# Performance work log

Hardware: AMD Instinct MI355X
Metric: run time of the kernel (lower is better)

## Reference

```python
import jax, jax.numpy as jnp
import numpy as np

N = 50000      # nodes
E = 800000     # edges (before self loops)
RNA, SS, H, G = 645, 6, 128, 200
EPS = 1e-5

def setup_inputs() -> dict:
    key = jax.random.key(0)
    ks = jax.random.split(key, 16)
    def rn(k, shape, s=0.05):
        return jax.random.normal(k, shape, jnp.float32) * s
    return {
        "rna_embeddings": jax.random.normal(ks[0], (N, RNA), jnp.float32),
        "ss_emb": jax.random.normal(ks[1], (N, SS), jnp.float32),
        "edge_index": jax.random.randint(ks[2], (2, E), 0, N),
        "batch": jnp.sort(jax.random.randint(ks[3], (N,), 0, G)),
        "W_fuse": rn(ks[4], (RNA + SS, H)), "b_fuse": jnp.zeros((H,), jnp.float32),
        "ln1_g": jnp.ones((H,), jnp.float32), "ln1_b": jnp.zeros((H,), jnp.float32),
        "W_gat": rn(ks[5], (H, H)), "att_src": rn(ks[6], (H,)), "att_dst": rn(ks[7], (H,)),
        "b_gat": jnp.zeros((H,), jnp.float32),
        "gn_w": jnp.ones((H,), jnp.float32), "gn_b": jnp.zeros((H,), jnp.float32), "gn_ms": jnp.ones((H,), jnp.float32),
        "W_gate": rn(ks[8], (2 * H, H)), "b_gate": jnp.zeros((H,), jnp.float32),
        "W_head": rn(ks[9], (H, H)), "b_head": jnp.zeros((H,), jnp.float32),
        "ln2_g": jnp.ones((H,), jnp.float32), "ln2_b": jnp.zeros((H,), jnp.float32),
        "W_fc1": rn(ks[10], (H, H // 2)), "b_fc1": jnp.zeros((H // 2,), jnp.float32),
        "ln3_g": jnp.ones((H // 2,), jnp.float32), "ln3_b": jnp.zeros((H // 2,), jnp.float32),
        "W_fc2": rn(ks[11], (H // 2, 1)), "b_fc2": jnp.zeros((1,), jnp.float32),
    }

def _ln(x, g, b):
    m = jnp.mean(x, -1, keepdims=True)
    v = jnp.mean(jnp.square(x - m), -1, keepdims=True)
    return (x - m) * jax.lax.rsqrt(v + EPS) * g + b

def _graphnorm(x, batch, w, b, ms):
    cnt = jax.ops.segment_sum(jnp.ones((x.shape[0], 1), x.dtype), batch, num_segments=G)
    mean = jax.ops.segment_sum(x, batch, num_segments=G) / jnp.maximum(cnt, 1.0)
    out = x - ms * mean[batch]
    var = jax.ops.segment_sum(jnp.square(out), batch, num_segments=G) / jnp.maximum(cnt, 1.0)
    std = jnp.sqrt(var + EPS)
    return w * out / std[batch] + b

def _gat(x, src, dst, W, a_src, a_dst, bias):
    xw = x @ W                                     # [N,H]
    e = (xw @ a_src)[src] + (xw @ a_dst)[dst]      # per-edge score
    e = jax.nn.leaky_relu(e, 0.2)
    m = jax.ops.segment_max(e, dst, num_segments=N)  # every dst has a self loop
    e = jnp.exp(e - m[dst])
    s = jax.ops.segment_sum(e, dst, num_segments=N)
    alpha = e / (s[dst] + 1e-16)
    return jax.ops.segment_sum(alpha[:, None] * xw[src], dst, num_segments=N) + bias

def reference(rna_embeddings, ss_emb, edge_index, batch,
              W_fuse, b_fuse, ln1_g, ln1_b,
              W_gat, att_src, att_dst, b_gat,
              gn_w, gn_b, gn_ms,
              W_gate, b_gate, W_head, b_head, ln2_g, ln2_b,
              W_fc1, b_fc1, ln3_g, ln3_b, W_fc2, b_fc2):
    loop = jnp.arange(N)
    src = jnp.concatenate([edge_index[0], loop])   # PyG GATConv add_self_loops=True
    dst = jnp.concatenate([edge_index[1], loop])
    h = jax.nn.relu(_ln(jnp.concatenate([rna_embeddings, ss_emb], -1) @ W_fuse + b_fuse, ln1_g, ln1_b))
    h_res = h
    h = jax.nn.relu(_graphnorm(_gat(h, src, dst, W_gat, att_src, att_dst, b_gat), batch, gn_w, gn_b, gn_ms))
    h1 = h
    h = jax.nn.relu(_graphnorm(_gat(h1, src, dst, W_gat, att_src, att_dst, b_gat), batch, gn_w, gn_b, gn_ms))
    h2 = h + h_res
    gate = jax.nn.sigmoid(jnp.concatenate([h1, h2], -1) @ W_gate + b_gate)
    h = gate * h1 + (1.0 - gate) * h2
    h = jax.nn.relu(_ln(h @ W_head + b_head, ln2_g, ln2_b))
    h = jax.nn.relu(_ln(h @ W_fc1 + b_fc1, ln3_g, ln3_b))
    return (h @ W_fc2 + b_fc2)[:, 0]
```

## Files before the change

### kernel.cpp

```cpp
#include <hip/hip_runtime.h>
#include <hip/hip_bf16.h>
#include <math.h>

#define NN 50000
#define EE 800000
#define RNA_D 645
#define KFUSE 651
#define KPACK 704
#define HD 128
#define GG 200
#define SAK 72
#define HGS 136

typedef __attribute__((ext_vector_type(8))) short shortx8;
typedef __attribute__((ext_vector_type(4))) float floatx4;

__device__ __forceinline__ float lrelu(float x){ return x >= 0.f ? x : 0.2f*x; }
__device__ __forceinline__ short f2bf(float x){
  union { __hip_bfloat16 h; short s; } u; u.h = __float2bfloat16(x); return u.s;
}
__device__ __forceinline__ float bf2f(short s){
  union { float f; unsigned u; } c; c.u = ((unsigned)(unsigned short)s) << 16; return c.f;
}
__device__ __forceinline__ float2 upk(unsigned u){
  union { float f; unsigned v; } a, b;
  a.v = u << 16; b.v = u & 0xffff0000u;
  return make_float2(a.f, b.f);
}

__global__ void hist_gstart_kernel(const int* __restrict__ dst, int* __restrict__ deg,
                                   const int* __restrict__ batch, int* __restrict__ gstart){
  int e = blockIdx.x*256 + threadIdx.x;
  if (e < EE) atomicAdd(&deg[dst[e]], 1);
  if (e < NN){
    int g = batch[e];
    if (e == 0){ for (int gg=0; gg<=g; ++gg) gstart[gg] = 0; }
    else { int gp = batch[e-1]; for (int gg=gp+1; gg<=g; ++gg) gstart[gg] = e; }
    if (e == NN-1){ for (int gg=g+1; gg<=GG; ++gg) gstart[gg] = NN; }
  }
}
__global__ void scan1_kernel(const int* __restrict__ deg, int* __restrict__ row_start,
                             int* __restrict__ blocksum){
  __shared__ int s[256];
  int i = blockIdx.x*256 + threadIdx.x;
  int v = (i < NN) ? deg[i] : 0;
  s[threadIdx.x] = v;
  __syncthreads();
  for (int off=1; off<256; off<<=1){
    int t = (threadIdx.x >= off) ? s[threadIdx.x-off] : 0;
    __syncthreads();
    s[threadIdx.x] += t;
    __syncthreads();
  }
  if (i < NN) row_start[i] = s[threadIdx.x] - v;
  if (threadIdx.x == 255) blocksum[blockIdx.x] = s[255];
}
__global__ void scan2_kernel(int* __restrict__ blocksum, int nb){
  __shared__ int s[256];
  int v = (threadIdx.x < nb) ? blocksum[threadIdx.x] : 0;
  s[threadIdx.x] = v;
  __syncthreads();
  for (int off=1; off<256; off<<=1){
    int t = (threadIdx.x >= off) ? s[threadIdx.x-off] : 0;
    __syncthreads();
    s[threadIdx.x] += t;
    __syncthreads();
  }
  blocksum[threadIdx.x] = s[threadIdx.x] - v;
}
__global__ void scan3_kernel(int* __restrict__ row_start, const int* __restrict__ blocksum,
                             int* __restrict__ cursor){
  int i = blockIdx.x*256 + threadIdx.x;
  if (i < NN){
    int v = row_start[i] + blocksum[blockIdx.x];
    row_start[i] = v;
    cursor[i] = v;
  }
  if (i == 0) row_start[NN] = EE;
}
__global__ void scatter_kernel(const int* __restrict__ srcl, const int* __restrict__ dstl,
                               int* __restrict__ cursor, int* __restrict__ csr_src){
  int e = blockIdx.x*256 + threadIdx.x;
  if (e >= EE) return;
  int d = dstl[e];
  int slot = atomicAdd(&cursor[d], 1);
  csr_src[slot] = srcl[e];
}

__global__ void wprep_all_kernel(const float* __restrict__ Wf, const float* __restrict__ Wg,
                                 const float* __restrict__ Wgt, const float* __restrict__ Wh,
                                 const float* __restrict__ W1,
                                 short* __restrict__ Tf, short* __restrict__ Tg,
                                 short* __restrict__ Tgt, short* __restrict__ Th,
                                 short* __restrict__ T1){
  int idx = blockIdx.x*256 + threadIdx.x;
  const int S0=128*KPACK, S1=128*128, S2=128*256, S3=128*128, S4=64*128;
  if (idx < S0){ int n=idx/KPACK, k=idx-n*KPACK; Tf[idx]=f2bf(k<KFUSE ? Wf[k*128+n] : 0.f); return; }
  idx -= S0;
  if (idx < S1){ int n=idx>>7, k=idx&127; Tg[idx]=f2bf(Wg[k*128+n]); return; }
  idx -= S1;
  if (idx < S2){ int n=idx>>8, k=idx&255; Tgt[idx]=f2bf(Wgt[k*128+n]); return; }
  idx -= S2;
  if (idx < S3){ int n=idx>>7, k=idx&127; Th[idx]=f2bf(Wh[k*128+n]); return; }
  idx -= S3;
  if (idx < S4){ int n=idx>>7, k=idx&127; T1[idx]=f2bf(W1[k*64+n]); return; }
}

__launch_bounds__(256)
__global__ void fuse_xw_kernel(const float* __restrict__ rna, const float* __restrict__ ss,
                               const short* __restrict__ Wtf, const float* __restrict__ bfu,
                               const float* __restrict__ g1, const float* __restrict__ b1,
                               const short* __restrict__ Wtg,
                               const float* __restrict__ as_, const float* __restrict__ ad_,
                               float* __restrict__ hout, short* __restrict__ xwb,
                               float* __restrict__ es, float* __restrict__ ed){
  __shared__ short sA[128*SAK];
  __shared__ short sB[128*SAK];
  __shared__ short hA[128*HGS];
  const int tid  = threadIdx.x;
  const int wave = tid >> 6, lane = tid & 63;
  const int quad = lane >> 4, l16 = lane & 15;
  const int rowBase = blockIdx.x * 128;
  const int srow = tid >> 1, shalf = tid & 1;
  const int sgr = rowBase + srow;

  floatx4 acc[2][8];
  #pragma unroll
  for (int t=0;t<2;++t)
    #pragma unroll
    for (int ct=0;ct<8;++ct)
      #pragma unroll
      for (int j=0;j<4;++j) acc[t][ct][j] = 0.f;

  for (int k0 = 0; k0 < KPACK; k0 += 64){
    {
      short tmp[32];
      if (sgr < NN && k0 < 640){
        const float* rrow = rna + (size_t)sgr*RNA_D + k0 + shalf*32;
        #pragma unroll
        for (int j=0;j<32;++j) tmp[j] = f2bf(rrow[j]);
      } else if (sgr < NN){
        int cb = k0 + shalf*32;
        #pragma unroll
        for (int j=0;j<32;++j){
          int c = cb + j;
          float v = 0.f;
          if (c < RNA_D) v = rna[(size_t)sgr*RNA_D + c];
          else if (c < KFUSE) v = ss[sgr*6 + (c - RNA_D)];
          tmp[j] = f2bf(v);
        }
      } else {
        #pragma unroll
        for (int j=0;j<32;++j) tmp[j] = 0;
      }
      #pragma unroll
      for (int q8=0;q8<4;++q8)
        *(shortx8*)&sA[srow*SAK + shalf*32 + q8*8] = *(shortx8*)&tmp[q8*8];
    }
    {
      int col = tid >> 1, kb = k0 + (tid&1)*32;
      #pragma unroll
      for (int q8=0;q8<4;++q8)
        *(shortx8*)&sB[col*SAK + (tid&1)*32 + q8*8] = *(const shortx8*)&Wtf[(size_t)col*KPACK + kb + q8*8];
    }
    __syncthreads();
    #pragma unroll
    for (int ks=0; ks<2; ++ks){
      int kb = ks*32 + quad*8;
      shortx8 af0 = *(const shortx8*)&sA[(wave*32 +      l16)*SAK + kb];
      shortx8 af1 = *(const shortx8*)&sA[(wave*32 + 16 + l16)*SAK + kb];
      #pragma unroll
      for (int ct=0; ct<8; ++ct){
        shortx8 bf = *(const shortx8*)&sB[(ct*16 + l16)*SAK + kb];
        acc[0][ct] = __builtin_amdgcn_mfma_f32_16x16x32_bf16(af0, bf, acc[0][ct], 0,0,0);
        acc[1][ct] = __builtin_amdgcn_mfma_f32_16x16x32_bf16(af1, bf, acc[1][ct], 0,0,0);
      }
    }
    __syncthreads();
  }

  {
    float biasv[8], gv[8], bv[8];
    #pragma unroll
    for (int ct=0;ct<8;++ct){
      biasv[ct] = bfu[ct*16+l16]; gv[ct] = g1[ct*16+l16]; bv[ct] = b1[ct*16+l16];
    }
    #pragma unroll
    for (int t=0;t<2;++t)
      #pragma unroll
      for (int i=0;i<4;++i){
        int row = wave*32 + t*16 + quad*4 + i;
        int gr = rowBase + row;
        float v[8]; float s=0.f, q=0.f;
        #pragma unroll
        for (int ct=0;ct<8;++ct){
          v[ct] = acc[t][ct][i] + biasv[ct];
          s += v[ct]; q = fmaf(v[ct], v[ct], q);
        }
        #pragma unroll
        for (int off=1; off<16; off<<=1){ s += __shfl_xor(s,off); q += __shfl_xor(q,off); }
        float mean = s * (1.f/128.f);
        float inv  = rsqrtf(q*(1.f/128.f) - mean*mean + 1e-5f);
        #pragma unroll
        for (int ct=0;ct<8;++ct){
          float o = fmaxf((v[ct]-mean)*inv*gv[ct] + bv[ct], 0.f);
          if (gr < NN) hout[(size_t)gr*HD + ct*16 + l16] = o;
          hA[row*HGS + ct*16 + l16] = f2bf(o);
        }
      }
  }
  __syncthreads();

  floatx4 acc2[2][8];
  #pragma unroll
  for (int t=0;t<2;++t)
    #pragma unroll
    for (int ct=0;ct<8;++ct)
      #pragma unroll
      for (int j=0;j<4;++j) acc2[t][ct][j] = 0.f;

  for (int c2=0; c2<2; ++c2){
    {
      int col = tid >> 1, kb2 = c2*64 + (tid&1)*32;
      #pragma unroll
      for (int q8=0;q8<4;++q8)
        *(shortx8*)&sB[col*SAK + (tid&1)*32 + q8*8] = *(const shortx8*)&Wtg[(size_t)col*HD + kb2 + q8*8];
    }
    __syncthreads();
    #pragma unroll
    for (int ks=0; ks<2; ++ks){
      int kg = c2*64 + ks*32 + quad*8;
      int kk = ks*32 + quad*8;
      shortx8 af0 = *(const shortx8*)&hA[(wave*32 +      l16)*HGS + kg];
      shortx8 af1 = *(const shortx8*)&hA[(wave*32 + 16 + l16)*HGS + kg];
      #pragma unroll
      for (int ct=0; ct<8; ++ct){
        shortx8 bf = *(const shortx8*)&sB[(ct*16 + l16)*SAK + kk];
        acc2[0][ct] = __builtin_amdgcn_mfma_f32_16x16x32_bf16(af0, bf, acc2[0][ct], 0,0,0);
        acc2[1][ct] = __builtin_amdgcn_mfma_f32_16x16x32_bf16(af1, bf, acc2[1][ct], 0,0,0);
      }
    }
    __syncthreads();
  }

  {
    float asv[8], adv[8];
    #pragma unroll
    for (int ct=0;ct<8;++ct){ asv[ct] = as_[ct*16+l16]; adv[ct] = ad_[ct*16+l16]; }
    #pragma unroll
    for (int t=0;t<2;++t)
      #pragma unroll
      for (int i=0;i<4;++i){
        int gr = rowBase + wave*32 + t*16 + quad*4 + i;
        float s=0.f, d=0.f;
        #pragma unroll
        for (int ct=0;ct<8;++ct){
          float v = acc2[t][ct][i];
          s = fmaf(v, asv[ct], s); d = fmaf(v, adv[ct], d);
          if (gr < NN) xwb[(size_t)gr*HD + ct*16 + l16] = f2bf(v);
        }
        #pragma unroll
        for (int off=1; off<16; off<<=1){ s += __shfl_xor(s,off); d += __shfl_xor(d,off); }
        if (l16 == 0 && gr < NN){ es[gr] = s; ed[gr] = d; }
      }
  }
}

template<int MODE, int NT, bool GNA>
__launch_bounds__(256)
__global__ void mfma_gemm(const float* __restrict__ A0,
                          const short* __restrict__ Apk,
                          const short* __restrict__ Wt, const float* __restrict__ bias,
                          const float* __restrict__ gw, const float* __restrict__ gb,
                          const float* __restrict__ as_, const float* __restrict__ ad_,
                          const int* __restrict__ batch, const float* __restrict__ gnsh,
                          const float* __restrict__ gnsc, float* __restrict__ side,
                          float* __restrict__ out, short* __restrict__ outb,
                          float* __restrict__ es, float* __restrict__ ed,
                          int K, int Kp){
  __shared__ short sA[128*SAK];
  __shared__ short sB[NT*16*SAK];
  const int tid  = threadIdx.x;
  const int wave = tid >> 6, lane = tid & 63;
  const int quad = lane >> 4, l16 = lane & 15;
  const int rowBase = blockIdx.x * 128;
  const int NCOL = NT*16;

  floatx4 acc[2][NT];
  #pragma unroll
  for (int t=0;t<2;++t)
    #pragma unroll
    for (int ct=0;ct<NT;++ct)
      #pragma unroll
      for (int j=0;j<4;++j) acc[t][ct][j] = 0.f;

  const int srow = tid >> 1, shalf = tid & 1;
  const int sgr = rowBase + srow;

  for (int k0 = 0; k0 < K; k0 += 64){
    {
      int kb = k0 + shalf*32;
      short tmp[32];
      if (GNA){
        int g = (sgr < NN) ? batch[sgr] : 0;
        const float* py  = A0 + (size_t)sgr*HD + kb;
        const float* psh = gnsh + g*HD + kb;
        const float* psc = gnsc + g*HD + kb;
        const float* pbb = gb + kb;
        #pragma unroll
        for (int q4=0;q4<8;++q4){
          float4 yv = (sgr < NN) ? *(const float4*)(py + q4*4) : make_float4(0.f,0.f,0.f,0.f);
          float4 sh = *(const float4*)(psh + q4*4);
          float4 sc = *(const float4*)(psc + q4*4);
          float4 bb = *(const float4*)(pbb + q4*4);
          float4 v;
          v.x = fmaxf((yv.x - sh.x)*sc.x + bb.x, 0.f);
          v.y = fmaxf((yv.y - sh.y)*sc.y + bb.y, 0.f);
          v.z = fmaxf((yv.z - sh.z)*sc.z + bb.z, 0.f);
          v.w = fmaxf((yv.w - sh.w)*sc.w + bb.w, 0.f);
          if (sgr < NN) *(float4*)&side[(size_t)sgr*HD + kb + q4*4] = v;
          tmp[q4*4+0]=f2bf(v.x); tmp[q4*4+1]=f2bf(v.y);
          tmp[q4*4+2]=f2bf(v.z); tmp[q4*4+3]=f2bf(v.w);
        }
      } else {
        const float* p = A0 + (size_t)sgr*HD + kb;
        #pragma unroll
        for (int q4=0;q4<8;++q4){
          float4 f = (sgr < NN) ? *(const float4*)(p + q4*4) : make_float4(0.f,0.f,0.f,0.f);
          tmp[q4*4+0]=f2bf(f.x); tmp[q4*4+1]=f2bf(f.y);
          tmp[q4*4+2]=f2bf(f.z); tmp[q4*4+3]=f2bf(f.w);
        }
      }
      #pragma unroll
      for (int q8=0;q8<4;++q8)
        *(shortx8*)&sA[srow*SAK + shalf*32 + q8*8] = *(shortx8*)&tmp[q8*8];
    }
    {
      int col = tid >> 1, kb = k0 + (tid&1)*32;
      #pragma unroll
      for (int q8=0;q8<4;++q8)
        *(shortx8*)&sB[col*SAK + (tid&1)*32 + q8*8] = *(const shortx8*)&Wt[(size_t)col*Kp + kb + q8*8];
    }
    __syncthreads();
    #pragma unroll
    for (int ks=0; ks<2; ++ks){
      int kb = ks*32 + quad*8;
      shortx8 af0 = *(const shortx8*)&sA[(wave*32 +      l16)*SAK + kb];
      shortx8 af1 = *(const shortx8*)&sA[(wave*32 + 16 + l16)*SAK + kb];
      #pragma unroll
      for (int ct=0; ct<NT; ++ct){
        shortx8 bf = *(const shortx8*)&sB[(ct*16 + l16)*SAK + kb];
        acc[0][ct] = __builtin_amdgcn_mfma_f32_16x16x32_bf16(af0, bf, acc[0][ct], 0,0,0);
        acc[1][ct] = __builtin_amdgcn_mfma_f32_16x16x32_bf16(af1, bf, acc[1][ct], 0,0,0);
      }
    }
    __syncthreads();
  }

  {
    float asv[NT], adv[NT];
    #pragma unroll
    for (int ct=0;ct<NT;++ct){ asv[ct] = as_[ct*16+l16]; adv[ct] = ad_[ct*16+l16]; }
    #pragma unroll
    for (int t=0;t<2;++t)
      #pragma unroll
      for (int i=0;i<4;++i){
        int gr = rowBase + wave*32 + t*16 + quad*4 + i;
        float s=0.f, d=0.f;
        #pragma unroll
        for (int ct=0;ct<NT;++ct){
          float v = acc[t][ct][i];
          s = fmaf(v, asv[ct], s); d = fmaf(v, adv[ct], d);
          if (gr < NN) outb[(size_t)gr*HD + ct*16 + l16] = f2bf(v);
        }
        #pragma unroll
        for (int off=1; off<16; off<<=1){ s += __shfl_xor(s,off); d += __shfl_xor(d,off); }
        if (l16 == 0 && gr < NN){ es[gr] = s; ed[gr] = d; }
      }
  }
}

__launch_bounds__(256)
__global__ void gat_aggregate_kernel(const short* __restrict__ xwb, const float* __restrict__ es,
                                     const float* __restrict__ ed, const int* __restrict__ row_start,
                                     const int* __restrict__ csr_src, const float* __restrict__ bgat,
                                     float* __restrict__ out){
  int gid = blockIdx.x*256 + threadIdx.x;
  int n = gid >> 6, lane = gid & 63;
  if (n >= NN) return;
  int beg = row_start[n], end = row_start[n+1];
  float edn = ed[n];
  float sc_self = lrelu(es[n] + edn);

  int i0 = beg + lane;
  bool v0 = i0 < end;
  int sA = v0 ? csr_src[i0] : 0;
  float eA = v0 ? lrelu(es[sA] + edn) : -3.0e38f;
  float m = fmaxf(sc_self, eA);
  for (int i = beg + 64 + lane; i < end; i += 64)
    m = fmaxf(m, lrelu(es[csr_src[i]] + edn));
  #pragma unroll
  for (int off=1; off<64; off<<=1) m = fmaxf(m, __shfl_xor(m, off));

  float wA = v0 ? __expf(eA - m) : 0.f;
  float wsum_l = wA;
  float wself = __expf(sc_self - m);
  float2 self2 = upk(*(const unsigned*)&xwb[(size_t)n*HD + 2*lane]);
  float a0 = wself*self2.x, a1 = wself*self2.y;

  int deg0 = min(end - beg, 64);
  int j = 0;
  for (; j + 8 <= deg0; j += 8){
    int ss[8]; float ww[8]; unsigned xv[8];
    #pragma unroll
    for (int u=0;u<8;++u){ ss[u]=__shfl(sA,j+u); ww[u]=__shfl(wA,j+u); }
    #pragma unroll
    for (int u=0;u<8;++u) xv[u] = *(const unsigned*)&xwb[(size_t)ss[u]*HD + 2*lane];
    #pragma unroll
    for (int u=0;u<8;++u){ float2 f=upk(xv[u]); a0=fmaf(ww[u],f.x,a0); a1=fmaf(ww[u],f.y,a1); }
  }
  for (; j < deg0; ++j){
    int s=__shfl(sA,j); float w=__shfl(wA,j);
    float2 f = upk(*(const unsigned*)&xwb[(size_t)s*HD + 2*lane]);
    a0=fmaf(w,f.x,a0); a1=fmaf(w,f.y,a1);
  }
  for (int c = beg + 64; c < end; c += 64){
    int i = c + lane;
    bool vb = i < end;
    int sB = vb ? csr_src[i] : 0;
    float wB = vb ? __expf(lrelu(es[sB] + edn) - m) : 0.f;
    wsum_l += wB;
    int degc = min(end - c, 64);
    for (int jj=0; jj<degc; ++jj){
      int s=__shfl(sB,jj); float w=__shfl(wB,jj);
      float2 f = upk(*(const unsigned*)&xwb[(size_t)s*HD + 2*lane]);
      a0=fmaf(w,f.x,a0); a1=fmaf(w,f.y,a1);
    }
  }
  #pragma unroll
  for (int off=1; off<64; off<<=1) wsum_l += __shfl_xor(wsum_l, off);
  float dinv = 1.f/(wsum_l + wself + 1e-16f);
  float2 b2 = *(const float2*)&bgat[2*lane];
  float2 o; o.x = a0*dinv + b2.x; o.y = a1*dinv + b2.y;
  *(float2*)&out[(size_t)n*HD + 2*lane] = o;
}

__launch_bounds__(1024)
__global__ void gn_group_kernel(const float* __restrict__ x, const int* __restrict__ gstart,
                                const float* __restrict__ gnw, const float* __restrict__ gnms,
                                float* __restrict__ shiftv, float* __restrict__ scalev){
  int g = blockIdx.x;
  int n0 = gstart[g], n1 = gstart[g+1];
  int f = threadIdx.x & 127, slot = threadIdx.x >> 7;
  float s = 0.f, q = 0.f;
  for (int n = n0 + slot; n < n1; n += 8){
    float v = x[(size_t)n*HD + f];
    s += v; q = fmaf(v, v, q);
  }
  __shared__ float rs[1024], rq[1024];
  rs[threadIdx.x] = s; rq[threadIdx.x] = q;
  __syncthreads();
  if (threadIdx.x < 512){ rs[threadIdx.x] += rs[threadIdx.x+512]; rq[threadIdx.x] += rq[threadIdx.x+512]; }
  __syncthreads();
  if (threadIdx.x < 256){ rs[threadIdx.x] += rs[threadIdx.x+256]; rq[threadIdx.x] += rq[threadIdx.x+256]; }
  __syncthreads();
  if (threadIdx.x < 128){
    s = rs[threadIdx.x] + rs[threadIdx.x+128];
    q = rq[threadIdx.x] + rq[threadIdx.x+128];
    float c = fmaxf((float)(n1 - n0), 1.f);
    float mean = s / c;
    float ms = gnms[f];
    float var = q/c - mean*mean*ms*(2.f - ms);
    shiftv[g*HD+f] = ms*mean;
    scalev[g*HD+f] = gnw[f] / sqrtf(var + 1e-5f);
  }
}

__launch_bounds__(256)
__global__ void tail_kernel(const float* __restrict__ h1, const float* __restrict__ y2,
                            const float* __restrict__ hres, const int* __restrict__ batch,
                            const float* __restrict__ gnsh, const float* __restrict__ gnsc,
                            const float* __restrict__ gnb,
                            const short* __restrict__ Wt_gate, const float* __restrict__ b_gate,
                            const short* __restrict__ Wt_head, const float* __restrict__ b_head,
                            const float* __restrict__ ln2g, const float* __restrict__ ln2b,
                            const short* __restrict__ Wt_fc1, const float* __restrict__ b_fc1,
                            const float* __restrict__ ln3g, const float* __restrict__ ln3b,
                            const float* __restrict__ W_fc2, const float* __restrict__ b_fc2,
                            float* __restrict__ outp){
  __shared__ short hgL[128*HGS];
  __shared__ short sA[128*SAK];
  __shared__ short sB[128*SAK];
  const int tid = threadIdx.x, wave = tid>>6, lane = tid&63;
  const int quad = lane>>4, l16 = lane&15;
  const int rowBase = blockIdx.x*128;
  const int srow = tid>>1, shalf = tid&1;
  const int sgr = rowBase + srow;

  floatx4 acc[2][8];
  #pragma unroll
  for (int t=0;t<2;++t)
    #pragma unroll
    for (int ct=0;ct<8;++ct)
      #pragma unroll
      for (int j=0;j<4;++j) acc[t][ct][j]=0.f;

  for (int c2=0; c2<4; ++c2){
    int kb = c2*64 + shalf*32;
    short tmp[32];
    if (kb < 128){
      const float* p = h1 + (size_t)sgr*HD + kb;
      #pragma unroll
      for (int q4=0;q4<8;++q4){
        float4 f = (sgr < NN) ? *(const float4*)(p + q4*4) : make_float4(0.f,0.f,0.f,0.f);
        tmp[q4*4+0]=f2bf(f.x); tmp[q4*4+1]=f2bf(f.y);
        tmp[q4*4+2]=f2bf(f.z); tmp[q4*4+3]=f2bf(f.w);
      }
    } else {
      int cb = kb - 128;
      int g = (sgr < NN) ? batch[sgr] : 0;
      const float* py  = y2   + (size_t)sgr*HD + cb;
      const float* ph  = hres + (size_t)sgr*HD + cb;
      const float* psh = gnsh + g*HD + cb;
      const float* psc = gnsc + g*HD + cb;
      const float* pbb = gnb + cb;
      #pragma unroll
      for (int q4=0;q4<8;++q4){
        float4 yv = (sgr < NN) ? *(const float4*)(py + q4*4) : make_float4(0.f,0.f,0.f,0.f);
        float4 hv = (sgr < NN) ? *(const float4*)(ph + q4*4) : make_float4(0.f,0.f,0.f,0.f);
        float4 sh = *(const float4*)(psh + q4*4);
        float4 sc = *(const float4*)(psc + q4*4);
        float4 bb = *(const float4*)(pbb + q4*4);
        float4 v;
        v.x = fmaxf((yv.x - sh.x)*sc.x + bb.x, 0.f) + hv.x;
        v.y = fmaxf((yv.y - sh.y)*sc.y + bb.y, 0.f) + hv.y;
        v.z = fmaxf((yv.z - sh.z)*sc.z + bb.z, 0.f) + hv.z;
        v.w = fmaxf((yv.w - sh.w)*sc.w + bb.w, 0.f) + hv.w;
        tmp[q4*4+0]=f2bf(v.x); tmp[q4*4+1]=f2bf(v.y);
        tmp[q4*4+2]=f2bf(v.z); tmp[q4*4+3]=f2bf(v.w);
      }
      #pragma unroll
      for (int q8=0;q8<4;++q8)
        *(shortx8*)&hgL[srow*HGS + cb + q8*8] = *(shortx8*)&tmp[q8*8];
    }
    #pragma unroll
    for (int q8=0;q8<4;++q8)
      *(shortx8*)&sA[srow*SAK + shalf*32 + q8*8] = *(shortx8*)&tmp[q8*8];
    {
      int col = tid >> 1, kb2 = c2*64 + (tid&1)*32;
      #pragma unroll
      for (int q8=0;q8<4;++q8)
        *(shortx8*)&sB[col*SAK + (tid&1)*32 + q8*8] = *(const shortx8*)&Wt_gate[(size_t)col*256 + kb2 + q8*8];
    }
    __syncthreads();
    #pragma unroll
    for (int ks=0; ks<2; ++ks){
      int kk = ks*32 + quad*8;
      shortx8 af0 = *(const shortx8*)&sA[(wave*32 +      l16)*SAK + kk];
      shortx8 af1 = *(const shortx8*)&sA[(wave*32 + 16 + l16)*SAK + kk];
      #pragma unroll
      for (int ct=0; ct<8; ++ct){
        shortx8 bf = *(const shortx8*)&sB[(ct*16 + l16)*SAK + kk];
        acc[0][ct] = __builtin_amdgcn_mfma_f32_16x16x32_bf16(af0, bf, acc[0][ct], 0,0,0);
        acc[1][ct] = __builtin_amdgcn_mfma_f32_16x16x32_bf16(af1, bf, acc[1][ct], 0,0,0);
      }
    }
    __syncthreads();
  }
  {
    float biasv[8];
    #pragma unroll
    for (int ct=0;ct<8;++ct) biasv[ct] = b_gate[ct*16+l16];
    #pragma unroll
    for (int t=0;t<2;++t)
      #pragma unroll
      for (int i=0;i<4;++i){
        int row = wave*32 + t*16 + quad*4 + i;
        int gr = rowBase + row;
        #pragma unroll
        for (int ct=0;ct<8;++ct){
          int c = ct*16 + l16;
          float g = 1.f/(1.f + __expf(-(acc[t][ct][i] + biasv[ct])));
          float x1 = (gr < NN) ? h1[(size_t)gr*HD + c] : 0.f;
          float x2 = bf2f(hgL[row*HGS + c]);
          hgL[row*HGS + c] = f2bf(g*x1 + (1.f-g)*x2);
        }
      }
  }
  __syncthreads();

  floatx4 acc2[2][8];
  #pragma unroll
  for (int t=0;t<2;++t)
    #pragma unroll
    for (int ct=0;ct<8;++ct)
      #pragma unroll
      for (int j=0;j<4;++j) acc2[t][ct][j]=0.f;
  for (int c2=0;c2<2;++c2){
    {
      int col = tid >> 1, kb2 = c2*64 + (tid&1)*32;
      #pragma unroll
      for (int q8=0;q8<4;++q8)
        *(shortx8*)&sB[col*SAK + (tid&1)*32 + q8*8] = *(const shortx8*)&Wt_head[(size_t)col*128 + kb2 + q8*8];
    }
    __syncthreads();
    #pragma unroll
    for (int ks=0; ks<2; ++ks){
      int kg = c2*64 + ks*32 + quad*8;
      int kk = ks*32 + quad*8;
      shortx8 af0 = *(const shortx8*)&hgL[(wave*32 +      l16)*HGS + kg];
      shortx8 af1 = *(const shortx8*)&hgL[(wave*32 + 16 + l16)*HGS + kg];
      #pragma unroll
      for (int ct=0; ct<8; ++ct){
        shortx8 bf = *(const shortx8*)&sB[(ct*16 + l16)*SAK + kk];
        acc2[0][ct] = __builtin_amdgcn_mfma_f32_16x16x32_bf16(af0, bf, acc2[0][ct], 0,0,0);
        acc2[1][ct] = __builtin_amdgcn_mfma_f32_16x16x32_bf16(af1, bf, acc2[1][ct], 0,0,0);
      }
    }
    __syncthreads();
  }
  {
    float biasv[8], gv[8], bv[8];
    #pragma unroll
    for (int ct=0;ct<8;++ct){
      biasv[ct] = b_head[ct*16+l16]; gv[ct] = ln2g[ct*16+l16]; bv[ct] = ln2b[ct*16+l16];
    }
    #pragma unroll
    for (int t=0;t<2;++t)
      #pragma unroll
      for (int i=0;i<4;++i){
        int row = wave*32 + t*16 + quad*4 + i;
        float v[8]; float s=0.f, q=0.f;
        #pragma unroll
        for (int ct=0;ct<8;++ct){
          v[ct] = acc2[t][ct][i] + biasv[ct];
          s += v[ct]; q = fmaf(v[ct], v[ct], q);
        }
        #pragma unroll
        for (int off=1; off<16; off<<=1){ s += __shfl_xor(s,off); q += __shfl_xor(q,off); }
        float mean = s * (1.f/128.f);
        float inv  = rsqrtf(q*(1.f/128.f) - mean*mean + 1e-5f);
        #pragma unroll
        for (int ct=0;ct<8;++ct)
          hgL[row*HGS + ct*16 + l16] = f2bf(fmaxf((v[ct]-mean)*inv*gv[ct] + bv[ct], 0.f));
      }
  }
  __syncthreads();

  floatx4 acc3[2][4];
  #pragma unroll
  for (int t=0;t<2;++t)
    #pragma unroll
    for (int ct=0;ct<4;++ct)
      #pragma unroll
      for (int j=0;j<4;++j) acc3[t][ct][j]=0.f;
  for (int c2=0;c2<2;++c2){
    if (tid < 128){
      int col = tid >> 1, kb2 = c2*64 + (tid&1)*32;
      #pragma unroll
      for (int q8=0;q8<4;++q8)
        *(shortx8*)&sB[col*SAK + (tid&1)*32 + q8*8] = *(const shortx8*)&Wt_fc1[(size_t)col*128 + kb2 + q8*8];
    }
    __syncthreads();
    #pragma unroll
    for (int ks=0; ks<2; ++ks){
      int kg = c2*64 + ks*32 + quad*8;
      int kk = ks*32 + quad*8;
      shortx8 af0 = *(const shortx8*)&hgL[(wave*32 +      l16)*HGS + kg];
      shortx8 af1 = *(const shortx8*)&hgL[(wave*32 + 16 + l16)*HGS + kg];
      #pragma unroll
      for (int ct=0; ct<4; ++ct){
        shortx8 bf = *(const shortx8*)&sB[(ct*16 + l16)*SAK + kk];
        acc3[0][ct] = __builtin_amdgcn_mfma_f32_16x16x32_bf16(af0, bf, acc3[0][ct], 0,0,0);
        acc3[1][ct] = __builtin_amdgcn_mfma_f32_16x16x32_bf16(af1, bf, acc3[1][ct], 0,0,0);
      }
    }
    __syncthreads();
  }
  {
    float biasv[4], gv[4], bv[4], w2v[4];
    #pragma unroll
    for (int ct=0;ct<4;++ct){
      biasv[ct] = b_fc1[ct*16+l16]; gv[ct] = ln3g[ct*16+l16]; bv[ct] = ln3b[ct*16+l16];
      w2v[ct] = W_fc2[ct*16+l16];
    }
    float b2 = b_fc2[0];
    #pragma unroll
    for (int t=0;t<2;++t)
      #pragma unroll
      for (int i=0;i<4;++i){
        int gr = rowBase + wave*32 + t*16 + quad*4 + i;
        float v[4]; float s=0.f, q=0.f;
        #pragma unroll
        for (int ct=0;ct<4;++ct){
          v[ct] = acc3[t][ct][i] + biasv[ct];
          s += v[ct]; q = fmaf(v[ct], v[ct], q);
        }
        #pragma unroll
        for (int off=1; off<16; off<<=1){ s += __shfl_xor(s,off); q += __shfl_xor(q,off); }
        float mean = s * (1.f/64.f);
        float inv  = rsqrtf(q*(1.f/64.f) - mean*mean + 1e-5f);
        float p = 0.f;
        #pragma unroll
        for (int ct=0;ct<4;++ct){
          float o = fmaxf((v[ct]-mean)*inv*gv[ct] + bv[ct], 0.f);
          p = fmaf(o, w2v[ct], p);
        }
        #pragma unroll
        for (int off=1; off<16; off<<=1) p += __shfl_xor(p, off);
        if (l16 == 0 && gr < NN) outp[gr] = p + b2;
      }
  }
}

extern "C" void kernel_launch(void* const* d_in, const int* in_sizes, int n_in,
                              void* d_out, int out_size, void* d_ws, size_t ws_size,
                              hipStream_t stream){
  const float* rna    = (const float*)d_in[0];
  const float* ss     = (const float*)d_in[1];
  const int*   eidx   = (const int*)d_in[2];
  const int*   batch  = (const int*)d_in[3];
  const float* W_fuse = (const float*)d_in[4];
  const float* b_fuse = (const float*)d_in[5];
  const float* ln1_g  = (const float*)d_in[6];
  const float* ln1_b  = (const float*)d_in[7];
  const float* W_gat  = (const float*)d_in[8];
  const float* att_src= (const float*)d_in[9];
  const float* att_dst= (const float*)d_in[10];
  const float* b_gat  = (const float*)d_in[11];
  const float* gn_w   = (const float*)d_in[12];
  const float* gn_b   = (const float*)d_in[13];
  const float* gn_ms  = (const float*)d_in[14];
  const float* W_gate = (const float*)d_in[15];
  const float* b_gate = (const float*)d_in[16];
  const float* W_head = (const float*)d_in[17];
  const float* b_head = (const float*)d_in[18];
  const float* ln2_g  = (const float*)d_in[19];
  const float* ln2_b  = (const float*)d_in[20];
  const float* W_fc1  = (const float*)d_in[21];
  const float* b_fc1  = (const float*)d_in[22];
  const float* ln3_g  = (const float*)d_in[23];
  const float* ln3_b  = (const float*)d_in[24];
  const float* W_fc2  = (const float*)d_in[25];
  const float* b_fc2  = (const float*)d_in[26];
  float* outp = (float*)d_out;

  const int* srcl = eidx;
  const int* dstl = eidx + EE;

  char* base = (char*)d_ws;
  size_t off = 0;
  auto alloc = [&](size_t bytes)->void*{
    void* p = base + off; off = (off + bytes + 255) & ~(size_t)255; return p;
  };
  float* h    = (float*)alloc((size_t)NN*HD*4);
  float* h1   = (float*)alloc((size_t)NN*HD*4);
  float* y    = (float*)alloc((size_t)NN*HD*4);
  short* xwb  = (short*)alloc((size_t)NN*HD*2);
  float* es   = (float*)alloc((size_t)NN*4);
  float* ed   = (float*)alloc((size_t)NN*4);
  float* shiftv = (float*)alloc(GG*HD*4);
  float* scalev = (float*)alloc(GG*HD*4);
  int* deg       = (int*)alloc((size_t)NN*4);
  int* row_start = (int*)alloc((size_t)(NN+1)*4);
  int* cursor    = (int*)alloc((size_t)NN*4);
  int* csr_src   = (int*)alloc((size_t)EE*4);
  int* blocksum  = (int*)alloc(256*4);
  int* gstart    = (int*)alloc((GG+1)*4);
  short* Wt_fuse = (short*)alloc((size_t)128*KPACK*2);
  short* Wt_gat  = (short*)alloc((size_t)128*128*2);
  short* Wt_gate = (short*)alloc((size_t)128*256*2);
  short* Wt_head = (short*)alloc((size_t)128*128*2);
  short* Wt_fc1  = (short*)alloc((size_t)64*128*2);

  const int NB  = (NN + 255)/256;
  const int GB  = (NN + 127)/128;
  const int EB  = (EE + 255)/256;
  const int WVB = (NN*64 + 255)/256;
  const int WPREP_TOT = 128*KPACK + 128*128 + 128*256 + 128*128 + 64*128;

  wprep_all_kernel<<<(WPREP_TOT+255)/256, 256, 0, stream>>>(
      W_fuse, W_gat, W_gate, W_head, W_fc1,
      Wt_fuse, Wt_gat, Wt_gate, Wt_head, Wt_fc1);

  hipMemsetAsync(deg, 0, (size_t)NN*4, stream);
  hist_gstart_kernel<<<EB, 256, 0, stream>>>(dstl, deg, batch, gstart);
  scan1_kernel<<<NB, 256, 0, stream>>>(deg, row_start, blocksum);
  scan2_kernel<<<1, 256, 0, stream>>>(blocksum, NB);
  scan3_kernel<<<NB, 256, 0, stream>>>(row_start, blocksum, cursor);
  scatter_kernel<<<EB, 256, 0, stream>>>(srcl, dstl, cursor, csr_src);

  fuse_xw_kernel<<<GB, 256, 0, stream>>>(rna, ss, Wt_fuse, b_fuse, ln1_g, ln1_b,
      Wt_gat, att_src, att_dst, h, xwb, es, ed);

  gat_aggregate_kernel<<<WVB, 256, 0, stream>>>(xwb, es, ed, row_start, csr_src, b_gat, y);
  gn_group_kernel<<<GG, 1024, 0, stream>>>(y, gstart, gn_w, gn_ms, shiftv, scalev);

  mfma_gemm<1,8,true><<<GB, 256, 0, stream>>>(y, nullptr, Wt_gat, nullptr, nullptr, gn_b,
      att_src, att_dst, batch, shiftv, scalev, h1, nullptr, xwb, es, ed, HD, HD);
  gat_aggregate_kernel<<<WVB, 256, 0, stream>>>(xwb, es, ed, row_start, csr_src, b_gat, y);
  gn_group_kernel<<<GG, 1024, 0, stream>>>(y, gstart, gn_w, gn_ms, shiftv, scalev);

  tail_kernel<<<GB, 256, 0, stream>>>(h1, y, h, batch, shiftv, scalev, gn_b,
      Wt_gate, b_gate, Wt_head, b_head, ln2_g, ln2_b,
      Wt_fc1, b_fc1, ln3_g, ln3_b, W_fc2, b_fc2, outp);
}
```

Baseline: 558.6 us.

## Coalesce global-to-LDS tile loads across GEMM kernels with lane-per-column mapping

Replaces the per-thread row-contiguous loads (each thread reading 32 consecutive floats of one row) with a mapping where each lane of a wave reads one column, so a wave reads a contiguous 64-float row segment in one coalesced access. Weight tiles are likewise loaded as 4-byte words with consecutive threads covering consecutive k. The aim is better global memory coalescing for the large rna embedding stream and the activation tiles. In exchange it uses scalar 2-byte LDS stores and narrower loads instead of 16-byte vector accesses, which adds instruction count and possible LDS bank conflicts. It also drops unused template and kernel parameters.

```diff
diff --git a/kernel.cpp b/kernel.cpp
--- a/kernel.cpp
+++ b/kernel.cpp
@@ -121,8 +121,9 @@
   const int wave = tid >> 6, lane = tid & 63;
   const int quad = lane >> 4, l16 = lane & 15;
   const int rowBase = blockIdx.x * 128;
-  const int srow = tid >> 1, shalf = tid & 1;
-  const int sgr = rowBase + srow;
+  const int cA = lane;
+  const int kk2 = (tid & 31)*2;
+  const int nb0 = tid >> 5;
 
   floatx4 acc[2][8];
   #pragma unroll
@@ -133,35 +134,34 @@
       for (int j=0;j<4;++j) acc[t][ct][j] = 0.f;
 
   for (int k0 = 0; k0 < KPACK; k0 += 64){
+    if (k0 < 640){
+      #pragma unroll
+      for (int i=0;i<32;++i){
+        int r = wave + i*4;
+        int gr = rowBase + r;
+        float v = (gr < NN) ? rna[(size_t)gr*RNA_D + k0 + cA] : 0.f;
+        sA[r*SAK + cA] = f2bf(v);
+      }
+    } else {
+      int c = k0 + cA;
+      #pragma unroll
+      for (int i=0;i<32;++i){
+        int r = wave + i*4;
+        int gr = rowBase + r;
+        float v = 0.f;
+        if (gr < NN){
+          if (c < RNA_D) v = rna[(size_t)gr*RNA_D + c];
+          else if (c < KFUSE) v = ss[gr*6 + (c - RNA_D)];
+        }
+        sA[r*SAK + cA] = f2bf(v);
+      }
+    }
     {
-      short tmp[32];
-      if (sgr < NN && k0 < 640){
-        const float* rrow = rna + (size_t)sgr*RNA_D + k0 + shalf*32;
-        #pragma unroll
-        for (int j=0;j<32;++j) tmp[j] = f2bf(rrow[j]);
-      } else if (sgr < NN){
-        int cb = k0 + shalf*32;
-        #pragma unroll
-        for (int j=0;j<32;++j){
-          int c = cb + j;
-          float v = 0.f;
-          if (c < RNA_D) v = rna[(size_t)sgr*RNA_D + c];
-          else if (c < KFUSE) v = ss[sgr*6 + (c - RNA_D)];
-          tmp[j] = f2bf(v);
-        }
-      } else {
-        #pragma unroll
-        for (int j=0;j<32;++j) tmp[j] = 0;
-      }
-      #pragma unroll
-      for (int q8=0;q8<4;++q8)
-        *(shortx8*)&sA[srow*SAK + shalf*32 + q8*8] = *(shortx8*)&tmp[q8*8];
-    }
-    {
-      int col = tid >> 1, kb = k0 + (tid&1)*32;
-      #pragma unroll
-      for (int q8=0;q8<4;++q8)
-        *(shortx8*)&sB[col*SAK + (tid&1)*32 + q8*8] = *(const shortx8*)&Wtf[(size_t)col*KPACK + kb + q8*8];
+      #pragma unroll
+      for (int i=0;i<16;++i){
+        int n = nb0 + i*8;
+        *(unsigned*)&sB[n*SAK + kk2] = *(const unsigned*)&Wtf[(size_t)n*KPACK + k0 + kk2];
+      }
     }
     __syncthreads();
     #pragma unroll
@@ -221,10 +221,11 @@
 
   for (int c2=0; c2<2; ++c2){
     {
-      int col = tid >> 1, kb2 = c2*64 + (tid&1)*32;
-      #pragma unroll
-      for (int q8=0;q8<4;++q8)
-        *(shortx8*)&sB[col*SAK + (tid&1)*32 + q8*8] = *(const shortx8*)&Wtg[(size_t)col*HD + kb2 + q8*8];
+      #pragma unroll
+      for (int i=0;i<16;++i){
+        int n = nb0 + i*8;
+        *(unsigned*)&sB[n*SAK + kk2] = *(const unsigned*)&Wtg[(size_t)n*HD + c2*64 + kk2];
+      }
     }
     __syncthreads();
     #pragma unroll
@@ -266,16 +267,15 @@
   }
 }
 
-template<int MODE, int NT, bool GNA>
+template<int NT, bool GNA>
 __launch_bounds__(256)
 __global__ void mfma_gemm(const float* __restrict__ A0,
-                          const short* __restrict__ Apk,
-                          const short* __restrict__ Wt, const float* __restrict__ bias,
-                          const float* __restrict__ gw, const float* __restrict__ gb,
+                          const short* __restrict__ Wt,
+                          const float* __restrict__ gb,
                           const float* __restrict__ as_, const float* __restrict__ ad_,
                           const int* __restrict__ batch, const float* __restrict__ gnsh,
                           const float* __restrict__ gnsc, float* __restrict__ side,
-                          float* __restrict__ out, short* __restrict__ outb,
+                          short* __restrict__ outb,
                           float* __restrict__ es, float* __restrict__ ed,
                           int K, int Kp){
   __shared__ short sA[128*SAK];
@@ -284,7 +284,9 @@
   const int wave = tid >> 6, lane = tid & 63;
   const int quad = lane >> 4, l16 = lane & 15;
   const int rowBase = blockIdx.x * 128;
-  const int NCOL = NT*16;
+  const int cA = lane;
+  const int kk2 = (tid & 31)*2;
+  const int nb0 = tid >> 5;
 
   floatx4 acc[2][NT];
   #pragma unroll
@@ -294,52 +296,31 @@
       #pragma unroll
       for (int j=0;j<4;++j) acc[t][ct][j] = 0.f;
 
-  const int srow = tid >> 1, shalf = tid & 1;
-  const int sgr = rowBase + srow;
-
   for (int k0 = 0; k0 < K; k0 += 64){
+    #pragma unroll
+    for (int i=0;i<32;++i){
+      int r = wave + i*4;
+      int gr = rowBase + r;
+      float v = 0.f;
+      if (GNA){
+        if (gr < NN){
+          int g = batch[gr];
+          float yv = A0[(size_t)gr*HD + k0 + cA];
+          float o = fmaxf((yv - gnsh[g*HD + k0 + cA])*gnsc[g*HD + k0 + cA] + gb[k0 + cA], 0.f);
+          side[(size_t)gr*HD + k0 + cA] = o;
+          v = o;
+        }
+      } else {
+        if (gr < NN) v = A0[(size_t)gr*HD + k0 + cA];
+      }
+      sA[r*SAK + cA] = f2bf(v);
+    }
     {
-      int kb = k0 + shalf*32;
-      short tmp[32];
-      if (GNA){
-        int g = (sgr < NN) ? batch[sgr] : 0;
-        const float* py  = A0 + (size_t)sgr*HD + kb;
-        const float* psh = gnsh + g*HD + kb;
-        const float* psc = gnsc + g*HD + kb;
-        const float* pbb = gb + kb;
-        #pragma unroll
-        for (int q4=0;q4<8;++q4){
-          float4 yv = (sgr < NN) ? *(const float4*)(py + q4*4) : make_float4(0.f,0.f,0.f,0.f);
-          float4 sh = *(const float4*)(psh + q4*4);
-          float4 sc = *(const float4*)(psc + q4*4);
-          float4 bb = *(const float4*)(pbb + q4*4);
-          float4 v;
-          v.x = fmaxf((yv.x - sh.x)*sc.x + bb.x, 0.f);
-          v.y = fmaxf((yv.y - sh.y)*sc.y + bb.y, 0.f);
-          v.z = fmaxf((yv.z - sh.z)*sc.z + bb.z, 0.f);
-          v.w = fmaxf((yv.w - sh.w)*sc.w + bb.w, 0.f);
-          if (sgr < NN) *(float4*)&side[(size_t)sgr*HD + kb + q4*4] = v;
-          tmp[q4*4+0]=f2bf(v.x); tmp[q4*4+1]=f2bf(v.y);
-          tmp[q4*4+2]=f2bf(v.z); tmp[q4*4+3]=f2bf(v.w);
-        }
-      } else {
-        const float* p = A0 + (size_t)sgr*HD + kb;
-        #pragma unroll
-        for (int q4=0;q4<8;++q4){
-          float4 f = (sgr < NN) ? *(const float4*)(p + q4*4) : make_float4(0.f,0.f,0.f,0.f);
-          tmp[q4*4+0]=f2bf(f.x); tmp[q4*4+1]=f2bf(f.y);
-          tmp[q4*4+2]=f2bf(f.z); tmp[q4*4+3]=f2bf(f.w);
-        }
-      }
-      #pragma unroll
-      for (int q8=0;q8<4;++q8)
-        *(shortx8*)&sA[srow*SAK + shalf*32 + q8*8] = *(shortx8*)&tmp[q8*8];
-    }
-    {
-      int col = tid >> 1, kb = k0 + (tid&1)*32;
-      #pragma unroll
-      for (int q8=0;q8<4;++q8)
-        *(shortx8*)&sB[col*SAK + (tid&1)*32 + q8*8] = *(const shortx8*)&Wt[(size_t)col*Kp + kb + q8*8];
+      #pragma unroll
+      for (int i=0;i<NT*2;++i){
+        int n = nb0 + i*8;
+        *(unsigned*)&sB[n*SAK + kk2] = *(const unsigned*)&Wt[(size_t)n*Kp + k0 + kk2];
+      }
     }
     __syncthreads();
     #pragma unroll
@@ -494,8 +475,9 @@
   const int tid = threadIdx.x, wave = tid>>6, lane = tid&63;
   const int quad = lane>>4, l16 = lane&15;
   const int rowBase = blockIdx.x*128;
-  const int srow = tid>>1, shalf = tid&1;
-  const int sgr = rowBase + srow;
+  const int cA = lane;
+  const int kk2 = (tid & 31)*2;
+  const int nb0 = tid >> 5;
 
   floatx4 acc[2][8];
   #pragma unroll
@@ -506,51 +488,39 @@
       for (int j=0;j<4;++j) acc[t][ct][j]=0.f;
 
   for (int c2=0; c2<4; ++c2){
-    int kb = c2*64 + shalf*32;
-    short tmp[32];
+    int kb = c2*64;
     if (kb < 128){
-      const float* p = h1 + (size_t)sgr*HD + kb;
-      #pragma unroll
-      for (int q4=0;q4<8;++q4){
-        float4 f = (sgr < NN) ? *(const float4*)(p + q4*4) : make_float4(0.f,0.f,0.f,0.f);
-        tmp[q4*4+0]=f2bf(f.x); tmp[q4*4+1]=f2bf(f.y);
-        tmp[q4*4+2]=f2bf(f.z); tmp[q4*4+3]=f2bf(f.w);
+      #pragma unroll
+      for (int i=0;i<32;++i){
+        int r = wave + i*4;
+        int gr = rowBase + r;
+        float v = (gr < NN) ? h1[(size_t)gr*HD + kb + cA] : 0.f;
+        sA[r*SAK + cA] = f2bf(v);
       }
     } else {
-      int cb = kb - 128;
-      int g = (sgr < NN) ? batch[sgr] : 0;
-      const float* py  = y2   + (size_t)sgr*HD + cb;
-      const float* ph  = hres + (size_t)sgr*HD + cb;
-      const float* psh = gnsh + g*HD + cb;
-      const float* psc = gnsc + g*HD + cb;
-      const float* pbb = gnb + cb;
-      #pragma unroll
-      for (int q4=0;q4<8;++q4){
-        float4 yv = (sgr < NN) ? *(const float4*)(py + q4*4) : make_float4(0.f,0.f,0.f,0.f);
-        float4 hv = (sgr < NN) ? *(const float4*)(ph + q4*4) : make_float4(0.f,0.f,0.f,0.f);
-        float4 sh = *(const float4*)(psh + q4*4);
-        float4 sc = *(const float4*)(psc + q4*4);
-        float4 bb = *(const float4*)(pbb + q4*4);
-        float4 v;
-        v.x = fmaxf((yv.x - sh.x)*sc.x + bb.x, 0.f) + hv.x;
-        v.y = fmaxf((yv.y - sh.y)*sc.y + bb.y, 0.f) + hv.y;
-        v.z = fmaxf((yv.z - sh.z)*sc.z + bb.z, 0.f) + hv.z;
-        v.w = fmaxf((yv.w - sh.w)*sc.w + bb.w, 0.f) + hv.w;
-        tmp[q4*4+0]=f2bf(v.x); tmp[q4*4+1]=f2bf(v.y);
-        tmp[q4*4+2]=f2bf(v.z); tmp[q4*4+3]=f2bf(v.w);
-      }
-      #pragma unroll
-      for (int q8=0;q8<4;++q8)
-        *(shortx8*)&hgL[srow*HGS + cb + q8*8] = *(shortx8*)&tmp[q8*8];
-    }
-    #pragma unroll
-    for (int q8=0;q8<4;++q8)
-      *(shortx8*)&sA[srow*SAK + shalf*32 + q8*8] = *(shortx8*)&tmp[q8*8];
+      int cb = kb - 128 + cA;
+      #pragma unroll
+      for (int i=0;i<32;++i){
+        int r = wave + i*4;
+        int gr = rowBase + r;
+        float v = 0.f;
+        if (gr < NN){
+          int g = batch[gr];
+          float yv = y2[(size_t)gr*HD + cb];
+          float hv = hres[(size_t)gr*HD + cb];
+          v = fmaxf((yv - gnsh[g*HD + cb])*gnsc[g*HD + cb] + gnb[cb], 0.f) + hv;
+        }
+        short bs = f2bf(v);
+        hgL[r*HGS + cb] = bs;
+        sA[r*SAK + cA] = bs;
+      }
+    }
     {
-      int col = tid >> 1, kb2 = c2*64 + (tid&1)*32;
-      #pragma unroll
-      for (int q8=0;q8<4;++q8)
-        *(shortx8*)&sB[col*SAK + (tid&1)*32 + q8*8] = *(const shortx8*)&Wt_gate[(size_t)col*256 + kb2 + q8*8];
+      #pragma unroll
+      for (int i=0;i<16;++i){
+        int n = nb0 + i*8;
+        *(unsigned*)&sB[n*SAK + kk2] = *(const unsigned*)&Wt_gate[(size_t)n*256 + kb + kk2];
+      }
     }
     __syncthreads();
     #pragma unroll
@@ -598,10 +568,11 @@
       for (int j=0;j<4;++j) acc2[t][ct][j]=0.f;
   for (int c2=0;c2<2;++c2){
     {
-      int col = tid >> 1, kb2 = c2*64 + (tid&1)*32;
-      #pragma unroll
-      for (int q8=0;q8<4;++q8)
-        *(shortx8*)&sB[col*SAK + (tid&1)*32 + q8*8] = *(const shortx8*)&Wt_head[(size_t)col*128 + kb2 + q8*8];
+      #pragma unroll
+      for (int i=0;i<16;++i){
+        int n = nb0 + i*8;
+        *(unsigned*)&sB[n*SAK + kk2] = *(const unsigned*)&Wt_head[(size_t)n*128 + c2*64 + kk2];
+      }
     }
     __syncthreads();
     #pragma unroll
@@ -655,11 +626,12 @@
       #pragma unroll
       for (int j=0;j<4;++j) acc3[t][ct][j]=0.f;
   for (int c2=0;c2<2;++c2){
-    if (tid < 128){
-      int col = tid >> 1, kb2 = c2*64 + (tid&1)*32;
-      #pragma unroll
-      for (int q8=0;q8<4;++q8)
-        *(shortx8*)&sB[col*SAK + (tid&1)*32 + q8*8] = *(const shortx8*)&Wt_fc1[(size_t)col*128 + kb2 + q8*8];
+    {
+      #pragma unroll
+      for (int i=0;i<8;++i){
+        int n = nb0 + i*8;
+        *(unsigned*)&sB[n*SAK + kk2] = *(const unsigned*)&Wt_fc1[(size_t)n*128 + c2*64 + kk2];
+      }
     }
     __syncthreads();
     #pragma unroll
@@ -796,8 +768,8 @@
   gat_aggregate_kernel<<<WVB, 256, 0, stream>>>(xwb, es, ed, row_start, csr_src, b_gat, y);
   gn_group_kernel<<<GG, 1024, 0, stream>>>(y, gstart, gn_w, gn_ms, shiftv, scalev);
 
-  mfma_gemm<1,8,true><<<GB, 256, 0, stream>>>(y, nullptr, Wt_gat, nullptr, nullptr, gn_b,
-      att_src, att_dst, batch, shiftv, scalev, h1, nullptr, xwb, es, ed, HD, HD);
+  mfma_gemm<8,true><<<GB, 256, 0, stream>>>(y, Wt_gat, gn_b,
+      att_src, att_dst, batch, shiftv, scalev, h1, xwb, es, ed, HD, HD);
   gat_aggregate_kernel<<<WVB, 256, 0, stream>>>(xwb, es, ed, row_start, csr_src, b_gat, y);
   gn_group_kernel<<<GG, 1024, 0, stream>>>(y, gstart, gn_w, gn_ms, shiftv, scalev);
 
```

After: 979.9 us. 1.75x slower.
